# Kernel optimization log

Hardware: AMD Instinct MI355X
Metric: run time of the kernel (lower is better)

## Reference

```python
import jax, jax.numpy as jnp
import numpy as np

B, S, D, H = 8, 1024, 1024, 16
DH = D // H  # 64


def setup_inputs() -> dict:
    key0 = jax.random.key(0)
    ks = jax.random.split(key0, 12)
    mk = lambda k, shape: jax.random.normal(k, shape, dtype=jnp.float32)
    inp = {
        "key": mk(ks[0], (B, S, D)),
        "value": mk(ks[1], (B, S, D)),
        "query": mk(ks[2], (B, S, D)),
        "mask": jax.random.randint(ks[3], (B, S, S), 0, 2).astype(jnp.bool_),
        "Wq": mk(ks[4], (D, D)) * 0.02, "bq": jnp.zeros((D,), jnp.float32),
        "Wk": mk(ks[5], (D, D)) * 0.02, "bk": jnp.zeros((D,), jnp.float32),
        "Wv": mk(ks[6], (D, D)) * 0.02, "bv": jnp.zeros((D,), jnp.float32),
        "Wo": mk(ks[7], (D, D)) * 0.02, "bo": jnp.zeros((D,), jnp.float32),
    }
    return inp


def _split_heads(x):
    # [B, S, D] -> [B, H, S, DH]
    return x.reshape(B, -1, H, DH).transpose(0, 2, 1, 3)


def reference(key, value, query, mask, Wq, bq, Wk, bk, Wv, bv, Wo, bo):
    # linear projections (nn.Linear: x @ W.T + b)
    q = _split_heads(query @ Wq.T + bq) / jnp.sqrt(jnp.float32(DH))
    k = _split_heads(key @ Wk.T + bk)
    v = _split_heads(value @ Wv.T + bv)
    # scores: [B, H, Q, K]
    scores = jnp.einsum("bhqd,bhkd->bhqk", q, k)
    scores = jnp.where(mask[:, None, :, :], jnp.float32(-1e18), scores)
    attn = jax.nn.softmax(scores, axis=-1)
    # dropout is identity in eval mode (deterministic reference)
    ctx = jnp.einsum("bhqk,bhkd->bhqd", attn, v)
    ctx = ctx.transpose(0, 2, 1, 3).reshape(B, -1, D)
    out = ctx @ Wo.T + bo
    return out, attn
```

## Files before the change

kernel.cpp:

```cpp
#include <hip/hip_runtime.h>
#include <hip/hip_bf16.h>

#define BB 8
#define SS 1024
#define DD 1024
#define HH 16
#define DHH 64
#define MM (BB*SS)

typedef __attribute__((ext_vector_type(8))) short short8;
typedef __attribute__((ext_vector_type(4))) float f32x4;
typedef __fp16 half2v __attribute__((ext_vector_type(2)));
typedef __fp16 half8 __attribute__((ext_vector_type(8)));

typedef __attribute__((address_space(3))) void lds_void;
typedef const __attribute__((address_space(1))) void gbl_void;

__device__ __forceinline__ unsigned short f2bf(float f) {
  union { __hip_bfloat16 b; unsigned short u; } cv;
  cv.b = __float2bfloat16(f);
  return cv.u;
}
__device__ __forceinline__ float bf2f(unsigned short u) {
  return __builtin_bit_cast(float, (unsigned)u << 16);
}

__global__ void k_conv_w(const float* __restrict__ in, unsigned short* __restrict__ out,
                         float scale, int n8) {
  int i = blockIdx.x * blockDim.x + threadIdx.x;
  if (i >= n8) return;
  const float4* in4 = (const float4*)in;
  float4 a = in4[i * 2];
  float4 b = in4[i * 2 + 1];
  unsigned int w[4];
  w[0] = f2bf(a.x * scale) | ((unsigned)f2bf(a.y * scale) << 16);
  w[1] = f2bf(a.z * scale) | ((unsigned)f2bf(a.w * scale) << 16);
  w[2] = f2bf(b.x * scale) | ((unsigned)f2bf(b.y * scale) << 16);
  w[3] = f2bf(b.z * scale) | ((unsigned)f2bf(b.w * scale) << 16);
  *(uint4*)(out + (size_t)i * 8) = *(uint4*)w;
}

__global__ void k_detect_mask(const unsigned int* __restrict__ m, int* __restrict__ flag) {
  if (threadIdx.x || blockIdx.x) return;
  int i32 = 1, f32m = 1;
  for (int i = 0; i < 64; ++i) {
    unsigned v = m[i];
    if (v > 1u) i32 = 0;
    if (v != 0u && v != 0x3F800000u) f32m = 0;
  }
  *flag = i32 ? 0 : (f32m ? 1 : 2);
}

__global__ void k_maskbits(const void* __restrict__ mask, const int* __restrict__ mmode,
                           unsigned short* __restrict__ out) {
  int i = blockIdx.x * blockDim.x + threadIdx.x;
  if (i >= BB * 32 * 64 * 32) return;
  int r = i & 31, cb = (i >> 5) & 63, qb = (i >> 11) & 31, b = i >> 16;
  size_t src = ((size_t)(b * SS + qb * 32 + r) * SS) + cb * 16;
  int mm = *mmode;
  unsigned short bits = 0;
  if (mm == 2) {
    const unsigned char* p = (const unsigned char*)mask + src;
    uint4 v = *(const uint4*)p;
    const unsigned char* bytes = (const unsigned char*)&v;
#pragma unroll
    for (int c = 0; c < 16; c++) bits |= (bytes[c] ? 1u : 0u) << c;
  } else {
    const unsigned int* p = (const unsigned int*)mask + src;
#pragma unroll
    for (int q = 0; q < 4; q++) {
      uint4 v = *(const uint4*)(p + q * 4);
      bits |= (v.x ? 1u : 0u) << (q * 4 + 0);
      bits |= (v.y ? 1u : 0u) << (q * 4 + 1);
      bits |= (v.z ? 1u : 0u) << (q * 4 + 2);
      bits |= (v.w ? 1u : 0u) << (q * 4 + 3);
    }
  }
  out[i] = bits;
}

__global__ void __launch_bounds__(256, 2) k_gemm_qkv(
    const unsigned short* __restrict__ Xq, const unsigned short* __restrict__ Xk,
    const unsigned short* __restrict__ Xv,
    const unsigned short* __restrict__ Wqb, const unsigned short* __restrict__ Wkb,
    const unsigned short* __restrict__ Wvb,
    const float* __restrict__ bq, const float* __restrict__ bk, const float* __restrict__ bv,
    unsigned short* __restrict__ Oq, unsigned short* __restrict__ Ok,
    unsigned short* __restrict__ Ov) {
  int bid = blockIdx.x;
  int by = bid & 63, bx = (bid >> 6) & 7, z = bid >> 9;
  const unsigned short* A = (z == 0) ? Xq : (z == 1 ? Xk : Xv);
  const unsigned short* W = (z == 0) ? Wqb : (z == 1 ? Wkb : Wvb);
  const float* bias = (z == 0) ? bq : (z == 1 ? bk : bv);
  float bsc = (z == 0) ? 0.125f : 1.0f;
  unsigned short* O = (z == 0) ? Oq : (z == 1 ? Ok : Ov);

  __shared__ alignas(16) unsigned char As[128 * 64 * 2];
  __shared__ alignas(16) unsigned char Bs[128 * 64 * 2];

  int t = threadIdx.x;
  int row0 = by * 128, col0 = bx * 128;
  int w = t >> 6, lane = t & 63, lr = lane & 15, lg = lane >> 4;
  int wm = w >> 1, wn = w & 1;

  int srow = w * 8 + (lane >> 3);
  int scol = (lane & 7) * 8;

  f32x4 z4 = {0.f, 0.f, 0.f, 0.f};
  f32x4 acc[4][4];
#pragma unroll
  for (int m = 0; m < 4; m++)
#pragma unroll
    for (int n = 0; n < 4; n++) acc[m][n] = z4;

  for (int kt = 0; kt < 16; ++kt) {
    int k0 = kt * 64;
#pragma unroll
    for (int i = 0; i < 4; ++i) {
      int r = i * 32 + srow;
      __builtin_amdgcn_global_load_lds(
          (gbl_void*)(A + (size_t)(row0 + r) * DD + k0 + scol),
          (lds_void*)(As + (i * 32 + w * 8) * 128), 16, 0, 0);
      __builtin_amdgcn_global_load_lds(
          (gbl_void*)(W + (size_t)(col0 + r) * DD + k0 + scol),
          (lds_void*)(Bs + (i * 32 + w * 8) * 128), 16, 0, 0);
    }
    __syncthreads();
#pragma unroll
    for (int kk = 0; kk < 2; ++kk) {
      short8 af[4], bfr[4];
#pragma unroll
      for (int m = 0; m < 4; m++) {
        int r = wm * 64 + m * 16 + lr;
        af[m] = *(const short8*)(As + r * 128 + kk * 64 + lg * 16);
      }
#pragma unroll
      for (int n = 0; n < 4; n++) {
        int r = wn * 64 + n * 16 + lr;
        bfr[n] = *(const short8*)(Bs + r * 128 + kk * 64 + lg * 16);
      }
#pragma unroll
      for (int m = 0; m < 4; m++)
#pragma unroll
        for (int n = 0; n < 4; n++)
          acc[m][n] = __builtin_amdgcn_mfma_f32_16x16x32_bf16(af[m], bfr[n], acc[m][n], 0, 0, 0);
    }
    __syncthreads();
  }
#pragma unroll
  for (int m = 0; m < 4; m++) {
#pragma unroll
    for (int n = 0; n < 4; n++) {
      int col = col0 + wn * 64 + n * 16 + lr;
      float bv_ = bias[col] * bsc;
#pragma unroll
      for (int j = 0; j < 4; j++) {
        int row = row0 + wm * 64 + m * 16 + lg * 4 + j;
        O[(size_t)row * DD + col] = f2bf(acc[m][n][j] + bv_);
      }
    }
  }
}

__global__ void __launch_bounds__(256, 2) k_gemm_out(
    const unsigned short* __restrict__ A, const unsigned short* __restrict__ W,
    const float* __restrict__ bias, float* __restrict__ Out) {
  __shared__ alignas(16) unsigned char As[128 * 64 * 2];
  __shared__ alignas(16) unsigned char Bs[128 * 64 * 2];

  int bid = blockIdx.x;
  int by = bid & 63, bx = bid >> 6;
  int t = threadIdx.x;
  int row0 = by * 128, col0 = bx * 128;
  int w = t >> 6, lane = t & 63, lr = lane & 15, lg = lane >> 4;
  int wm = w >> 1, wn = w & 1;

  int srow = w * 8 + (lane >> 3);
  int scol = (lane & 7) * 8;

  f32x4 z4 = {0.f, 0.f, 0.f, 0.f};
  f32x4 acc[4][4];
#pragma unroll
  for (int m = 0; m < 4; m++)
#pragma unroll
    for (int n = 0; n < 4; n++) acc[m][n] = z4;

  for (int kt = 0; kt < 16; ++kt) {
    int k0 = kt * 64;
#pragma unroll
    for (int i = 0; i < 4; ++i) {
      int r = i * 32 + srow;
      __builtin_amdgcn_global_load_lds(
          (gbl_void*)(A + (size_t)(row0 + r) * DD + k0 + scol),
          (lds_void*)(As + (i * 32 + w * 8) * 128), 16, 0, 0);
      __builtin_amdgcn_global_load_lds(
          (gbl_void*)(W + (size_t)(col0 + r) * DD + k0 + scol),
          (lds_void*)(Bs + (i * 32 + w * 8) * 128), 16, 0, 0);
    }
    __syncthreads();
#pragma unroll
    for (int kk = 0; kk < 2; ++kk) {
      short8 af[4], bfr[4];
#pragma unroll
      for (int m = 0; m < 4; m++) {
        int r = wm * 64 + m * 16 + lr;
        af[m] = *(const short8*)(As + r * 128 + kk * 64 + lg * 16);
      }
#pragma unroll
      for (int n = 0; n < 4; n++) {
        int r = wn * 64 + n * 16 + lr;
        bfr[n] = *(const short8*)(Bs + r * 128 + kk * 64 + lg * 16);
      }
#pragma unroll
      for (int m = 0; m < 4; m++)
#pragma unroll
        for (int n = 0; n < 4; n++)
          acc[m][n] = __builtin_amdgcn_mfma_f32_16x16x32_bf16(af[m], bfr[n], acc[m][n], 0, 0, 0);
    }
    __syncthreads();
  }
#pragma unroll
  for (int m = 0; m < 4; m++) {
#pragma unroll
    for (int n = 0; n < 4; n++) {
      int col = col0 + wn * 64 + n * 16 + lr;
      float bv_ = bias[col];
#pragma unroll
      for (int j = 0; j < 4; j++) {
        int row = row0 + wm * 64 + m * 16 + lg * 4 + j;
        Out[(size_t)row * DD + col] = acc[m][n][j] + bv_;
      }
    }
  }
}

__global__ void k_transpose_v(const unsigned short* __restrict__ V,
                              unsigned short* __restrict__ VT) {
  int blk = blockIdx.x;
  int s0 = (blk & 15) * 64;
  int h = (blk >> 4) & 15;
  int b = blk >> 8;
  __shared__ alignas(16) unsigned short T[64][72];
  int t = threadIdx.x;
  int rr = t >> 3, cc = t & 7;
#pragma unroll
  for (int p = 0; p < 2; p++) {
    int r = p * 32 + rr;
    uint4 v = *(const uint4*)(V + (size_t)(b * SS + s0 + r) * DD + h * 64 + cc * 8);
    *(uint4*)(&T[r][cc * 8]) = v;
  }
  __syncthreads();
#pragma unroll
  for (int p = 0; p < 2; p++) {
    int dh = p * 32 + rr;
    unsigned short tmp[8];
#pragma unroll
    for (int i = 0; i < 8; i++) tmp[i] = T[cc * 8 + i][dh];
    unsigned outw[4];
#pragma unroll
    for (int i = 0; i < 4; i++) {
      half2v hp = __builtin_amdgcn_cvt_pkrtz(bf2f(tmp[2 * i]), bf2f(tmp[2 * i + 1]));
      outw[i] = __builtin_bit_cast(unsigned, hp);
    }
    *(uint4*)(VT + (size_t)((b * HH + h) * DHH + dh) * SS + s0 + cc * 8) = *(uint4*)outw;
  }
}

__global__ void __launch_bounds__(256) k_attn(
    const unsigned short* __restrict__ Q, const unsigned short* __restrict__ K,
    const unsigned short* __restrict__ VT, const unsigned short* __restrict__ mbits,
    float* __restrict__ attn, unsigned short* __restrict__ ctx) {
  int wg = blockIdx.x;
  int xcd = wg & 7, idx = wg >> 3;
  int p_bh = xcd + (idx >> 5) * 8;
  int qb = idx & 31;
  int b = p_bh >> 4, h = p_bh & 15;
  int q0 = qb * 32;
  int t = threadIdx.x, w = t >> 6, lane = t & 63, lr = lane & 15, lg = lane >> 4;

  __shared__ float redsum[4][32];
  __shared__ alignas(16) unsigned char pbuf[24576];
  unsigned short (*P)[32][72] = (unsigned short(*)[32][72])pbuf;
  float (*cred)[32][64] = (float(*)[32][64])pbuf;

  short8 qf[2][2];
#pragma unroll
  for (int m = 0; m < 2; m++)
#pragma unroll
    for (int kb = 0; kb < 2; kb++)
      qf[m][kb] = *(const short8*)(Q + (size_t)(b * SS + q0 + m * 16 + lr) * DD +
                                   h * 64 + kb * 32 + lg * 8);

  const unsigned short* mb = mbits + (size_t)(b * 32 + qb) * 64 * 32;

  f32x4 z4 = {0.f, 0.f, 0.f, 0.f};
  float ps[2][4];
#pragma unroll
  for (int m = 0; m < 2; m++)
#pragma unroll
    for (int j = 0; j < 4; j++) ps[m][j] = 0.f;

  half2v scp[2][16][2];
#pragma unroll
  for (int c = 0; c < 16; c++) {
    int colb = w * 256 + c * 16;
    const unsigned short* kp = K + (size_t)(b * SS + colb + lr) * DD + h * 64 + lg * 8;
    short8 kf0 = *(const short8*)kp;
    short8 kf1 = *(const short8*)(kp + 32);
    int cb = w * 16 + c;
#pragma unroll
    for (int m = 0; m < 2; m++) {
      __builtin_amdgcn_s_setprio(1);
      f32x4 s = __builtin_amdgcn_mfma_f32_16x16x32_bf16(qf[m][0], kf0, z4, 0, 0, 0);
      s = __builtin_amdgcn_mfma_f32_16x16x32_bf16(qf[m][1], kf1, s, 0, 0, 0);
      __builtin_amdgcn_s_setprio(0);
      const unsigned short* mrow = mb + cb * 32 + m * 16 + lg * 4;
      ushort4 mw = *(const ushort4*)mrow;
      unsigned short mwa[4] = {mw.x, mw.y, mw.z, mw.w};
      float p[4];
#pragma unroll
      for (int j = 0; j < 4; j++)
        p[j] = ((mwa[j] >> lr) & 1) ? 0.0f : __expf(fminf(s[j], 10.0f));
      half2v h0 = __builtin_amdgcn_cvt_pkrtz(p[0], p[1]);
      half2v h1 = __builtin_amdgcn_cvt_pkrtz(p[2], p[3]);
      scp[m][c][0] = h0;
      scp[m][c][1] = h1;
      ps[m][0] += (float)h0[0];
      ps[m][1] += (float)h0[1];
      ps[m][2] += (float)h1[0];
      ps[m][3] += (float)h1[1];
    }
  }
#pragma unroll
  for (int m = 0; m < 2; m++)
#pragma unroll
    for (int j = 0; j < 4; j++) {
      float v = ps[m][j];
      v += __shfl_xor(v, 1);
      v += __shfl_xor(v, 2);
      v += __shfl_xor(v, 4);
      v += __shfl_xor(v, 8);
      ps[m][j] = v;
    }
  if (lr == 0) {
#pragma unroll
    for (int m = 0; m < 2; m++)
#pragma unroll
      for (int j = 0; j < 4; j++) redsum[w][m * 16 + lg * 4 + j] = ps[m][j];
  }
  __syncthreads();
  float inv[2][4];
#pragma unroll
  for (int m = 0; m < 2; m++)
#pragma unroll
    for (int j = 0; j < 4; j++) {
      int r = m * 16 + lg * 4 + j;
      inv[m][j] = 1.f / (redsum[0][r] + redsum[1][r] + redsum[2][r] + redsum[3][r]);
    }
  float invr[4];
#pragma unroll
  for (int rg = 0; rg < 4; rg++) {
    int r = rg * 8 + (lane >> 3);
    invr[rg] = 1.f / (redsum[0][r] + redsum[1][r] + redsum[2][r] + redsum[3][r]);
  }

  float* ab = attn + (size_t)((b * HH + h) * SS + q0) * SS;
  f32x4 cacc[2][4];
#pragma unroll
  for (int m = 0; m < 2; m++)
#pragma unroll
    for (int nb = 0; nb < 4; nb++) cacc[m][nb] = z4;

#pragma unroll
  for (int ch = 0; ch < 4; ch++) {
#pragma unroll
    for (int cc = 0; cc < 4; cc++) {
      int c = ch * 4 + cc;
      int col = cc * 16 + lr;
#pragma unroll
      for (int m = 0; m < 2; m++) {
        unsigned u0 = __builtin_bit_cast(unsigned, scp[m][c][0]);
        unsigned u1 = __builtin_bit_cast(unsigned, scp[m][c][1]);
        int r0 = m * 16 + lg * 4;
        P[w][r0 + 0][col] = (unsigned short)(u0 & 0xffffu);
        P[w][r0 + 1][col] = (unsigned short)(u0 >> 16);
        P[w][r0 + 2][col] = (unsigned short)(u1 & 0xffffu);
        P[w][r0 + 3][col] = (unsigned short)(u1 >> 16);
      }
    }
#pragma unroll
    for (int rg = 0; rg < 4; rg++) {
      int row = rg * 8 + (lane >> 3);
      float iv = invr[rg];
#pragma unroll
      for (int ci = 0; ci < 2; ci++) {
        int col = (lane & 7) * 4 + ci * 32;
        ushort4 hv = *(const ushort4*)(&P[w][row][col]);
        f32x4 o;
        o[0] = (float)__builtin_bit_cast(__fp16, hv.x) * iv;
        o[1] = (float)__builtin_bit_cast(__fp16, hv.y) * iv;
        o[2] = (float)__builtin_bit_cast(__fp16, hv.z) * iv;
        o[3] = (float)__builtin_bit_cast(__fp16, hv.w) * iv;
        __builtin_nontemporal_store(o, (f32x4*)(ab + (size_t)row * SS + w * 256 + ch * 64 + col));
      }
    }
#pragma unroll
    for (int kb = 0; kb < 2; kb++) {
      half8 vf[4];
#pragma unroll
      for (int nb = 0; nb < 4; nb++)
        vf[nb] = __builtin_bit_cast(half8,
            *(const short8*)(VT + (size_t)((b * HH + h) * DHH + nb * 16 + lr) * SS +
                             w * 256 + ch * 64 + kb * 32 + lg * 8));
      half8 pa[2];
#pragma unroll
      for (int m = 0; m < 2; m++)
        pa[m] = __builtin_bit_cast(half8, *(const short8*)(&P[w][m * 16 + lr][kb * 32 + lg * 8]));
      __builtin_amdgcn_s_setprio(1);
#pragma unroll
      for (int m = 0; m < 2; m++)
#pragma unroll
        for (int nb = 0; nb < 4; nb++)
          cacc[m][nb] = __builtin_amdgcn_mfma_f32_16x16x32_f16(pa[m], vf[nb], cacc[m][nb], 0, 0, 0);
      __builtin_amdgcn_s_setprio(0);
    }
  }
  __syncthreads();
  if (w > 0) {
#pragma unroll
    for (int m = 0; m < 2; m++)
#pragma unroll
      for (int nb = 0; nb < 4; nb++)
#pragma unroll
        for (int j = 0; j < 4; j++)
          cred[w - 1][m * 16 + lg * 4 + j][nb * 16 + lr] = cacc[m][nb][j];
  }
  __syncthreads();
  if (w == 0) {
#pragma unroll
    for (int m = 0; m < 2; m++)
#pragma unroll
      for (int nb = 0; nb < 4; nb++) {
        int col = nb * 16 + lr;
#pragma unroll
        for (int j = 0; j < 4; j++) {
          int rl = m * 16 + lg * 4 + j;
          float v = (cacc[m][nb][j] + cred[0][rl][col] + cred[1][rl][col] + cred[2][rl][col]) *
                    inv[m][j];
          ctx[(size_t)(b * SS + q0 + rl) * DD + h * 64 + col] = f2bf(v);
        }
      }
  }
}

extern "C" void kernel_launch(void* const* d_in, const int* in_sizes, int n_in,
                              void* d_out, int out_size, void* d_ws, size_t ws_size,
                              hipStream_t stream) {
  const float* key   = (const float*)d_in[0];
  const float* value = (const float*)d_in[1];
  const float* query = (const float*)d_in[2];
  const void*  mask  = d_in[3];
  const float* Wq = (const float*)d_in[4];
  const float* bq = (const float*)d_in[5];
  const float* Wk = (const float*)d_in[6];
  const float* bk = (const float*)d_in[7];
  const float* Wv = (const float*)d_in[8];
  const float* bv = (const float*)d_in[9];
  const float* Wo = (const float*)d_in[10];
  const float* bo = (const float*)d_in[11];

  unsigned short* wq_b = (unsigned short*)d_ws;
  unsigned short* wk_b = wq_b + (size_t)DD * DD;
  unsigned short* wv_b = wk_b + (size_t)DD * DD;
  unsigned short* wo_b = wv_b + (size_t)DD * DD;
  unsigned short* Qb   = wo_b + (size_t)DD * DD;
  unsigned short* Kb   = Qb + (size_t)MM * DD;
  unsigned short* Vb   = Kb + (size_t)MM * DD;
  unsigned short* VTb  = Vb + (size_t)MM * DD;
  unsigned short* CTXb = VTb + (size_t)MM * DD;
  unsigned short* MB   = CTXb + (size_t)MM * DD;
  int* flag = (int*)(MB + (size_t)BB * 32 * 64 * 32);
  size_t needed = (size_t)(4 * DD * DD + 5 * MM * DD) * 2 + (1u << 20) + 256;
  if (ws_size < needed) return;

  float* out  = (float*)d_out;
  float* attn = out + (size_t)MM * DD;

  unsigned short* Xq_b = (unsigned short*)attn;
  unsigned short* Xk_b = Xq_b + (size_t)MM * DD;
  unsigned short* Xv_b = Xk_b + (size_t)MM * DD;

  k_conv_w<<<512, 256, 0, stream>>>(Wq, wq_b, 0.125f, DD * DD / 8);
  k_conv_w<<<512, 256, 0, stream>>>(Wk, wk_b, 1.0f, DD * DD / 8);
  k_conv_w<<<512, 256, 0, stream>>>(Wv, wv_b, 1.0f, DD * DD / 8);
  k_conv_w<<<512, 256, 0, stream>>>(Wo, wo_b, 1.0f, DD * DD / 8);
  k_conv_w<<<4096, 256, 0, stream>>>(query, Xq_b, 1.0f, MM * DD / 8);
  k_conv_w<<<4096, 256, 0, stream>>>(key,   Xk_b, 1.0f, MM * DD / 8);
  k_conv_w<<<4096, 256, 0, stream>>>(value, Xv_b, 1.0f, MM * DD / 8);
  k_detect_mask<<<1, 1, 0, stream>>>((const unsigned int*)mask, flag);
  k_maskbits<<<2048, 256, 0, stream>>>(mask, flag, MB);
  k_gemm_qkv<<<1536, 256, 0, stream>>>(Xq_b, Xk_b, Xv_b, wq_b, wk_b, wv_b,
                                       bq, bk, bv, Qb, Kb, Vb);
  k_transpose_v<<<2048, 256, 0, stream>>>(Vb, VTb);
  k_attn<<<4096, 256, 0, stream>>>(Qb, Kb, VTb, MB, attn, CTXb);
  k_gemm_out<<<512, 256, 0, stream>>>(CTXb, wo_b, bo, out);
}
```

Measured before the change: 349.4 us.

## Fuse fp32 activation conversion into QKV GEMM and drop setprio hints

```diff
diff --git a/kernel.cpp b/kernel.cpp
--- a/kernel.cpp
+++ b/kernel.cpp
@@ -40,6 +40,21 @@
   *(uint4*)(out + (size_t)i * 8) = *(uint4*)w;
 }
 
+__global__ void k_conv_w_h(const float* __restrict__ in, unsigned short* __restrict__ out,
+                           float scale, int n8) {
+  int i = blockIdx.x * blockDim.x + threadIdx.x;
+  if (i >= n8) return;
+  const float4* in4 = (const float4*)in;
+  float4 a = in4[i * 2];
+  float4 b = in4[i * 2 + 1];
+  unsigned int w[4];
+  w[0] = __builtin_bit_cast(unsigned, __builtin_amdgcn_cvt_pkrtz(a.x * scale, a.y * scale));
+  w[1] = __builtin_bit_cast(unsigned, __builtin_amdgcn_cvt_pkrtz(a.z * scale, a.w * scale));
+  w[2] = __builtin_bit_cast(unsigned, __builtin_amdgcn_cvt_pkrtz(b.x * scale, b.y * scale));
+  w[3] = __builtin_bit_cast(unsigned, __builtin_amdgcn_cvt_pkrtz(b.z * scale, b.w * scale));
+  *(uint4*)(out + (size_t)i * 8) = *(uint4*)w;
+}
+
 __global__ void k_detect_mask(const unsigned int* __restrict__ m, int* __restrict__ flag) {
   if (threadIdx.x || blockIdx.x) return;
   int i32 = 1, f32m = 1;
@@ -80,22 +95,21 @@
 }
 
 __global__ void __launch_bounds__(256, 2) k_gemm_qkv(
-    const unsigned short* __restrict__ Xq, const unsigned short* __restrict__ Xk,
-    const unsigned short* __restrict__ Xv,
-    const unsigned short* __restrict__ Wqb, const unsigned short* __restrict__ Wkb,
-    const unsigned short* __restrict__ Wvb,
+    const float* __restrict__ Xq, const float* __restrict__ Xk, const float* __restrict__ Xv,
+    const unsigned short* __restrict__ Wqh, const unsigned short* __restrict__ Wkh,
+    const unsigned short* __restrict__ Wvh,
     const float* __restrict__ bq, const float* __restrict__ bk, const float* __restrict__ bv,
     unsigned short* __restrict__ Oq, unsigned short* __restrict__ Ok,
     unsigned short* __restrict__ Ov) {
   int bid = blockIdx.x;
   int by = bid & 63, bx = (bid >> 6) & 7, z = bid >> 9;
-  const unsigned short* A = (z == 0) ? Xq : (z == 1 ? Xk : Xv);
-  const unsigned short* W = (z == 0) ? Wqb : (z == 1 ? Wkb : Wvb);
+  const float* A = (z == 0) ? Xq : (z == 1 ? Xk : Xv);
+  const unsigned short* W = (z == 0) ? Wqh : (z == 1 ? Wkh : Wvh);
   const float* bias = (z == 0) ? bq : (z == 1 ? bk : bv);
   float bsc = (z == 0) ? 0.125f : 1.0f;
   unsigned short* O = (z == 0) ? Oq : (z == 1 ? Ok : Ov);
 
-  __shared__ alignas(16) unsigned char As[128 * 64 * 2];
+  __shared__ alignas(16) unsigned char As[128 * 64 * 4];
   __shared__ alignas(16) unsigned char Bs[128 * 64 * 2];
 
   int t = threadIdx.x;
@@ -103,9 +117,6 @@
   int w = t >> 6, lane = t & 63, lr = lane & 15, lg = lane >> 4;
   int wm = w >> 1, wn = w & 1;
 
-  int srow = w * 8 + (lane >> 3);
-  int scol = (lane & 7) * 8;
-
   f32x4 z4 = {0.f, 0.f, 0.f, 0.f};
   f32x4 acc[4][4];
 #pragma unroll
@@ -113,37 +124,52 @@
 #pragma unroll
     for (int n = 0; n < 4; n++) acc[m][n] = z4;
 
+  int arow = lane >> 4, acol = (lane & 15) * 4;
+  int brow = lane >> 3, bcol = (lane & 7) * 8;
+
   for (int kt = 0; kt < 16; ++kt) {
     int k0 = kt * 64;
 #pragma unroll
+    for (int i = 0; i < 8; ++i) {
+      int r = i * 16 + w * 4 + arow;
+      __builtin_amdgcn_global_load_lds(
+          (gbl_void*)(A + (size_t)(row0 + r) * DD + k0 + acol),
+          (lds_void*)(As + (i * 16 + w * 4) * 256), 16, 0, 0);
+    }
+#pragma unroll
     for (int i = 0; i < 4; ++i) {
-      int r = i * 32 + srow;
+      int r = i * 32 + w * 8 + brow;
       __builtin_amdgcn_global_load_lds(
-          (gbl_void*)(A + (size_t)(row0 + r) * DD + k0 + scol),
-          (lds_void*)(As + (i * 32 + w * 8) * 128), 16, 0, 0);
-      __builtin_amdgcn_global_load_lds(
-          (gbl_void*)(W + (size_t)(col0 + r) * DD + k0 + scol),
+          (gbl_void*)(W + (size_t)(col0 + r) * DD + k0 + bcol),
           (lds_void*)(Bs + (i * 32 + w * 8) * 128), 16, 0, 0);
     }
     __syncthreads();
 #pragma unroll
     for (int kk = 0; kk < 2; ++kk) {
-      short8 af[4], bfr[4];
+      half8 af[4], bfr[4];
 #pragma unroll
       for (int m = 0; m < 4; m++) {
         int r = wm * 64 + m * 16 + lr;
-        af[m] = *(const short8*)(As + r * 128 + kk * 64 + lg * 16);
+        const unsigned char* base = As + r * 256 + kk * 128 + lg * 32;
+        f32x4 lo = *(const f32x4*)base;
+        f32x4 hi = *(const f32x4*)(base + 16);
+        uint4 uu;
+        uu.x = __builtin_bit_cast(unsigned, __builtin_amdgcn_cvt_pkrtz(lo[0], lo[1]));
+        uu.y = __builtin_bit_cast(unsigned, __builtin_amdgcn_cvt_pkrtz(lo[2], lo[3]));
+        uu.z = __builtin_bit_cast(unsigned, __builtin_amdgcn_cvt_pkrtz(hi[0], hi[1]));
+        uu.w = __builtin_bit_cast(unsigned, __builtin_amdgcn_cvt_pkrtz(hi[2], hi[3]));
+        af[m] = __builtin_bit_cast(half8, uu);
       }
 #pragma unroll
       for (int n = 0; n < 4; n++) {
         int r = wn * 64 + n * 16 + lr;
-        bfr[n] = *(const short8*)(Bs + r * 128 + kk * 64 + lg * 16);
+        bfr[n] = __builtin_bit_cast(half8, *(const short8*)(Bs + r * 128 + kk * 64 + lg * 16));
       }
 #pragma unroll
       for (int m = 0; m < 4; m++)
 #pragma unroll
         for (int n = 0; n < 4; n++)
-          acc[m][n] = __builtin_amdgcn_mfma_f32_16x16x32_bf16(af[m], bfr[n], acc[m][n], 0, 0, 0);
+          acc[m][n] = __builtin_amdgcn_mfma_f32_16x16x32_f16(af[m], bfr[n], acc[m][n], 0, 0, 0);
     }
     __syncthreads();
   }
@@ -310,10 +336,8 @@
     int cb = w * 16 + c;
 #pragma unroll
     for (int m = 0; m < 2; m++) {
-      __builtin_amdgcn_s_setprio(1);
       f32x4 s = __builtin_amdgcn_mfma_f32_16x16x32_bf16(qf[m][0], kf0, z4, 0, 0, 0);
       s = __builtin_amdgcn_mfma_f32_16x16x32_bf16(qf[m][1], kf1, s, 0, 0, 0);
-      __builtin_amdgcn_s_setprio(0);
       const unsigned short* mrow = mb + cb * 32 + m * 16 + lg * 4;
       ushort4 mw = *(const ushort4*)mrow;
       unsigned short mwa[4] = {mw.x, mw.y, mw.z, mw.w};
@@ -416,13 +440,11 @@
 #pragma unroll
       for (int m = 0; m < 2; m++)
         pa[m] = __builtin_bit_cast(half8, *(const short8*)(&P[w][m * 16 + lr][kb * 32 + lg * 8]));
-      __builtin_amdgcn_s_setprio(1);
 #pragma unroll
       for (int m = 0; m < 2; m++)
 #pragma unroll
         for (int nb = 0; nb < 4; nb++)
           cacc[m][nb] = __builtin_amdgcn_mfma_f32_16x16x32_f16(pa[m], vf[nb], cacc[m][nb], 0, 0, 0);
-      __builtin_amdgcn_s_setprio(0);
     }
   }
   __syncthreads();
@@ -469,10 +491,10 @@
   const float* Wo = (const float*)d_in[10];
   const float* bo = (const float*)d_in[11];
 
-  unsigned short* wq_b = (unsigned short*)d_ws;
-  unsigned short* wk_b = wq_b + (size_t)DD * DD;
-  unsigned short* wv_b = wk_b + (size_t)DD * DD;
-  unsigned short* wo_b = wv_b + (size_t)DD * DD;
+  unsigned short* wq_h = (unsigned short*)d_ws;
+  unsigned short* wk_h = wq_h + (size_t)DD * DD;
+  unsigned short* wv_h = wk_h + (size_t)DD * DD;
+  unsigned short* wo_b = wv_h + (size_t)DD * DD;
   unsigned short* Qb   = wo_b + (size_t)DD * DD;
   unsigned short* Kb   = Qb + (size_t)MM * DD;
   unsigned short* Vb   = Kb + (size_t)MM * DD;
@@ -486,20 +508,13 @@
   float* out  = (float*)d_out;
   float* attn = out + (size_t)MM * DD;
 
-  unsigned short* Xq_b = (unsigned short*)attn;
-  unsigned short* Xk_b = Xq_b + (size_t)MM * DD;
-  unsigned short* Xv_b = Xk_b + (size_t)MM * DD;
-
-  k_conv_w<<<512, 256, 0, stream>>>(Wq, wq_b, 0.125f, DD * DD / 8);
-  k_conv_w<<<512, 256, 0, stream>>>(Wk, wk_b, 1.0f, DD * DD / 8);
-  k_conv_w<<<512, 256, 0, stream>>>(Wv, wv_b, 1.0f, DD * DD / 8);
+  k_conv_w_h<<<512, 256, 0, stream>>>(Wq, wq_h, 0.125f, DD * DD / 8);
+  k_conv_w_h<<<512, 256, 0, stream>>>(Wk, wk_h, 1.0f, DD * DD / 8);
+  k_conv_w_h<<<512, 256, 0, stream>>>(Wv, wv_h, 1.0f, DD * DD / 8);
   k_conv_w<<<512, 256, 0, stream>>>(Wo, wo_b, 1.0f, DD * DD / 8);
-  k_conv_w<<<4096, 256, 0, stream>>>(query, Xq_b, 1.0f, MM * DD / 8);
-  k_conv_w<<<4096, 256, 0, stream>>>(key,   Xk_b, 1.0f, MM * DD / 8);
-  k_conv_w<<<4096, 256, 0, stream>>>(value, Xv_b, 1.0f, MM * DD / 8);
   k_detect_mask<<<1, 1, 0, stream>>>((const unsigned int*)mask, flag);
   k_maskbits<<<2048, 256, 0, stream>>>(mask, flag, MB);
-  k_gemm_qkv<<<1536, 256, 0, stream>>>(Xq_b, Xk_b, Xv_b, wq_b, wk_b, wv_b,
+  k_gemm_qkv<<<1536, 256, 0, stream>>>(query, key, value, wq_h, wk_h, wv_h,
                                        bq, bk, bv, Qb, Kb, Vb);
   k_transpose_v<<<2048, 256, 0, stream>>>(Vb, VTb);
   k_attn<<<4096, 256, 0, stream>>>(Qb, Kb, VTb, MB, attn, CTXb);
```

Result: slower. 362.1 us (+3.6%).
